# Optimization experiments

Measured on AMD Instinct MI355X. Metric: run time of the kernel, lower is better.

## Reference

```python
import jax, jax.numpy as jnp
import numpy as np
from jax import lax

EPS = 1e-5
DIM = 384
HEADS = 12
EXPAND = 3  # head_expand -> DLA hidden = 36
HID = HEADS * EXPAND
MLP_HID = 4 * DIM


def layernorm(x, g, b):
    m = x.mean(-1, keepdims=True)
    v = jnp.var(x, axis=-1, keepdims=True)
    return (x - m) / jnp.sqrt(v + EPS) * g + b


def bn2d(x, g, b):
    # training-mode BatchNorm2d: biased batch stats over (N,H,W) per channel
    m = x.mean((0, 2, 3), keepdims=True)
    v = jnp.var(x, axis=(0, 2, 3), keepdims=True)
    return (x - m) / jnp.sqrt(v + EPS) * g[None, :, None, None] + b[None, :, None, None]


def setup_inputs() -> dict:
    key = jax.random.key(0)
    ks = jax.random.split(key, 12)
    d = {}
    d["x"] = jax.random.normal(ks[0], (32, 197, DIM), dtype=jnp.float32)
    d["ln1_g"] = jnp.ones((DIM,), jnp.float32)
    d["ln1_b"] = jnp.zeros((DIM,), jnp.float32)
    d["qkv_w"] = jax.random.normal(ks[1], (3 * DIM, DIM), jnp.float32) * 0.02
    # DLA conv_exapnd: 1x1 expand -> dw3x3 -> 1x1 project, each with BN
    d["conv_exp_w"] = jax.random.normal(ks[2], (HID, HEADS), jnp.float32) * 0.1
    d["bn1_g"] = jnp.ones((HID,), jnp.float32)
    d["bn1_b"] = jnp.zeros((HID,), jnp.float32)
    d["dw_w"] = jax.random.normal(ks[3], (HID, 1, 3, 3), jnp.float32) * 0.1
    d["bn2_g"] = jnp.ones((HID,), jnp.float32)
    d["bn2_b"] = jnp.zeros((HID,), jnp.float32)
    d["conv_pro_w"] = jax.random.normal(ks[4], (HEADS, HID), jnp.float32) * 0.1
    d["bn3_g"] = jnp.ones((HEADS,), jnp.float32)
    d["bn3_b"] = jnp.zeros((HEADS,), jnp.float32)
    d["abn_g"] = jnp.ones((HEADS,), jnp.float32)
    d["abn_b"] = jnp.zeros((HEADS,), jnp.float32)
    d["proj_w"] = jax.random.normal(ks[5], (DIM, DIM), jnp.float32) * 0.02
    d["proj_b"] = jnp.zeros((DIM,), jnp.float32)
    d["ln2_g"] = jnp.ones((DIM,), jnp.float32)
    d["ln2_b"] = jnp.zeros((DIM,), jnp.float32)
    d["fc1_w"] = jax.random.normal(ks[6], (MLP_HID, DIM), jnp.float32) * 0.02
    d["fc1_b"] = jnp.zeros((MLP_HID,), jnp.float32)
    d["fc2_w"] = jax.random.normal(ks[7], (DIM, MLP_HID), jnp.float32) * 0.02
    d["fc2_b"] = jnp.zeros((DIM,), jnp.float32)
    d["scale_ch"] = 1e-5 * jnp.ones((DIM,), jnp.float32)
    return d


def reference(x, ln1_g, ln1_b, qkv_w, conv_exp_w, bn1_g, bn1_b, dw_w, bn2_g, bn2_b,
              conv_pro_w, bn3_g, bn3_b, abn_g, abn_b, proj_w, proj_b,
              ln2_g, ln2_b, fc1_w, fc1_b, fc2_w, fc2_b, scale_ch):
    B, N, C = x.shape
    H = HEADS
    hd = C // H
    scale = hd ** -0.5
    sq = scale ** 0.5  # math.sqrt(self.scale) applied to q and k

    h = layernorm(x * 0.5, ln1_g, ln1_b)  # adjust_ratio = 0.5
    qkv = (h @ qkv_w.T).reshape(B, N, 3, H, hd).transpose(2, 0, 3, 1, 4)  # [3,B,H,N,hd]
    q, k, v = qkv[0] * sq, qkv[1] * sq, qkv[2]

    attn = jax.nn.softmax(jnp.einsum('bhnd,bhmd->bhnm', q, k), axis=-1)  # [B,H,N,N]

    # DLA conv_exapnd refine (stride 1, inp==oup -> residual)
    a0 = attn
    a = jnp.einsum('oi,bihw->bohw', conv_exp_w, attn)
    a = jnp.clip(bn2d(a, bn1_g, bn1_b), 0.0, 6.0)  # ReLU6
    a = lax.conv_general_dilated(a, dw_w, (1, 1), 'SAME',
                                 dimension_numbers=('NCHW', 'OIHW', 'NCHW'),
                                 feature_group_count=HID)
    a = jnp.clip(bn2d(a, bn2_g, bn2_b), 0.0, 6.0)
    a = jnp.einsum('oi,bihw->bohw', conv_pro_w, a)
    a = bn2d(a, bn3_g, bn3_b) + a0
    attn = bn2d(a, abn_g, abn_b)  # adapt_bn

    out = jnp.einsum('bhnm,bhmd->bhnd', attn, v).transpose(0, 2, 1, 3).reshape(B, N, C)
    out = out @ proj_w.T + proj_b
    x = x + out / 0.5

    m = layernorm(x * 0.5, ln2_g, ln2_b)
    m = jax.nn.gelu(m @ fc1_w.T + fc1_b, approximate=False)
    m = (m @ fc2_w.T + fc2_b) * scale_ch
    x = x + m / 0.5
    return x, attn
```

## Files before the change

### kernel.cpp

```cpp
#include <hip/hip_runtime.h>
#include <math.h>

#define EPS   1e-5f
#define NSEQ  197
#define DIM   384
#define NH    12
#define HD    32
#define MLPH  1536
#define NN2   38809
#define NROWS 6304
#define NPIX  1241888
#define XSIZE 2420736
#define SQF   0.4204482076268572f

typedef __bf16 bf16;
typedef __attribute__((ext_vector_type(2))) __fp16 fp16x2;
typedef __attribute__((ext_vector_type(2))) float floatx2;
typedef __attribute__((ext_vector_type(8))) __bf16 bf16x8;
typedef __attribute__((ext_vector_type(4))) float floatx4;
typedef unsigned int u32;
typedef const __attribute__((address_space(1))) u32* gptr_t;
typedef __attribute__((address_space(3))) u32* lptr_t;

#define ST_MOMSUM  0
#define ST_MOMPROD 16
#define ST_SC1     160
#define ST_SH1     200
#define ST_S2      256
#define ST_SS2     2560
#define ST_SC2     4864
#define ST_SH2     4900
#define ST_P3      4992
#define ST_ABG     8832
#define ST_TOTAL   8896

#define O_HB    0ull
#define O_Q     1228800ull
#define O_K     3649536ull
#define O_V     6070272ull
#define O_ATT0  8491008ull
#define O_X1    23393664ull
#define O_WQKV  25814400ull
#define O_WPRJ  26035584ull
#define O_WFC1  26109312ull
#define O_WFC2  26404224ull
#define O_STATS 26699136ull
#define WS_FLOATS (O_STATS + ST_TOTAL)
#define O_SBUF  (O_STATS + ST_TOTAL)
#define SBUF_WORDS 22353984ull
#define WS_FLOATS_MID (O_SBUF + SBUF_WORDS)

__device__ __forceinline__ u32 pack2(float a, float b) {
    u32 ua = __builtin_bit_cast(u32, a);
    u32 ub = __builtin_bit_cast(u32, b);
    return (ua >> 16) | (ub & 0xffff0000u);
}
__device__ __forceinline__ float unpk_lo(u32 w) { return __builtin_bit_cast(float, w << 16); }
__device__ __forceinline__ float unpk_hi(u32 w) { return __builtin_bit_cast(float, w & 0xffff0000u); }

__device__ __forceinline__ u32 packh2(float a, float b) {
    fp16x2 h = __builtin_amdgcn_cvt_pkrtz(a, b);
    return __builtin_bit_cast(u32, h);
}
__device__ __forceinline__ float unph_lo(u32 w) {
    fp16x2 h = __builtin_bit_cast(fp16x2, w);
    return (float)h.x;
}
__device__ __forceinline__ float unph_hi(u32 w) {
    fp16x2 h = __builtin_bit_cast(fp16x2, w);
    return (float)h.y;
}

template <int CTRL>
__device__ __forceinline__ float dpp_addf(float v) {
    int x = __builtin_amdgcn_update_dpp(0, __builtin_bit_cast(int, v),
                                        CTRL, 0xF, 0xF, true);
    return v + __builtin_bit_cast(float, x);
}
__device__ __forceinline__ float red16(float v) {
    v = dpp_addf<0xB1>(v);
    v = dpp_addf<0x4E>(v);
    v = dpp_addf<0x141>(v);
    v = dpp_addf<0x140>(v);
    return v;
}

template <int CTRL>
__device__ __forceinline__ u32 dpp_addh(u32 v) {
    int x = __builtin_amdgcn_update_dpp(0, __builtin_bit_cast(int, v),
                                        CTRL, 0xF, 0xF, true);
    fp16x2 a = __builtin_bit_cast(fp16x2, v);
    fp16x2 b = __builtin_bit_cast(fp16x2, (u32)x);
    fp16x2 c = a + b;
    return __builtin_bit_cast(u32, c);
}
__device__ __forceinline__ u32 red16h(u32 v) {
    v = dpp_addh<0xB1>(v);
    v = dpp_addh<0x4E>(v);
    v = dpp_addh<0x141>(v);
    v = dpp_addh<0x140>(v);
    return v;
}

__global__ __launch_bounds__(256) void k_cvt(const float* __restrict__ s0,
                                             const float* __restrict__ s1,
                                             const float* __restrict__ s2,
                                             const float* __restrict__ s3,
                                             bf16* __restrict__ d0,
                                             bf16* __restrict__ d1,
                                             bf16* __restrict__ d2,
                                             bf16* __restrict__ d3) {
    const int w = blockIdx.y;
    const float* s = (w == 0) ? s0 : (w == 1) ? s1 : (w == 2) ? s2 : s3;
    bf16* d = (w == 0) ? d0 : (w == 1) ? d1 : (w == 2) ? d2 : d3;
    const int n = (w == 0) ? 442368 : (w == 1) ? 147456 : 589824;
    for (int i = blockIdx.x * 256 + threadIdx.x; i < n; i += gridDim.x * 256)
        d[i] = (bf16)s[i];
}

__global__ __launch_bounds__(384) void k_ln(const float* __restrict__ xin,
                                            const float* __restrict__ g,
                                            const float* __restrict__ bb,
                                            bf16* __restrict__ hout) {
    const int r = blockIdx.x;
    const int t = threadIdx.x;
    float v = xin[(size_t)r * DIM + t] * 0.5f;
    float s = v, sq = v * v;
#pragma unroll
    for (int off = 32; off >= 1; off >>= 1) {
        s  += __shfl_xor(s, off);
        sq += __shfl_xor(sq, off);
    }
    __shared__ float ls[6], lq[6];
    __shared__ float mv[2];
    const int wid = t >> 6;
    if ((t & 63) == 0) { ls[wid] = s; lq[wid] = sq; }
    __syncthreads();
    if (t == 0) {
        float S = 0.f, Q = 0.f;
        for (int i = 0; i < 6; ++i) { S += ls[i]; Q += lq[i]; }
        float m = S / (float)DIM;
        mv[0] = m;
        mv[1] = rsqrtf(Q / (float)DIM - m * m + EPS);
    }
    __syncthreads();
    hout[(size_t)r * DIM + t] = (bf16)((v - mv[0]) * mv[1] * g[t] + bb[t]);
}

template <int KDIM>
__device__ __forceinline__ void mgemm(const bf16* __restrict__ A,
                                      const bf16* __restrict__ B,
                                      int row0, int col0,
                                      floatx4 (&acc)[4][4]) {
    __shared__ bf16 As[128 * 32];
    __shared__ bf16 Bs[128 * 32];
    const int tid = threadIdx.x;
    const int lane = tid & 63, wave = tid >> 6;
    const int wy = wave >> 1, wx = wave & 1;
    const int quad = lane >> 4, l15 = lane & 15;
    for (int k0 = 0; k0 < KDIM; k0 += 32) {
#pragma unroll
        for (int i = 0; i < 2; ++i) {
            const int e = (i * 256 + tid) * 8;
            const int r = e >> 5, kk = e & 31;
            __builtin_amdgcn_global_load_lds(
                (gptr_t)(A + (size_t)(row0 + r) * KDIM + k0 + kk),
                (lptr_t)(As + e), 16, 0, 0);
            __builtin_amdgcn_global_load_lds(
                (gptr_t)(B + (size_t)(col0 + r) * KDIM + k0 + kk),
                (lptr_t)(Bs + e), 16, 0, 0);
        }
        __syncthreads();
        bf16x8 af[4], bfr[4];
#pragma unroll
        for (int mi = 0; mi < 4; ++mi)
            af[mi] = *(const bf16x8*)&As[(wy * 64 + mi * 16 + l15) * 32 + quad * 8];
#pragma unroll
        for (int ni = 0; ni < 4; ++ni)
            bfr[ni] = *(const bf16x8*)&Bs[(wx * 64 + ni * 16 + l15) * 32 + quad * 8];
#pragma unroll
        for (int mi = 0; mi < 4; ++mi)
#pragma unroll
            for (int ni = 0; ni < 4; ++ni)
                acc[mi][ni] = __builtin_amdgcn_mfma_f32_16x16x32_bf16(
                    af[mi], bfr[ni], acc[mi][ni], 0, 0, 0);
        __syncthreads();
    }
}

__global__ __launch_bounds__(256) void k_qkv(const bf16* __restrict__ h,
                                             const bf16* __restrict__ w,
                                             bf16* __restrict__ qb,
                                             bf16* __restrict__ kxb,
                                             float* __restrict__ v) {
    floatx4 acc[4][4] = {};
    const int row0 = blockIdx.y * 128, col0 = blockIdx.x * 128;
    mgemm<DIM>(h, w, row0, col0, acc);
    const int lane = threadIdx.x & 63, wave = threadIdx.x >> 6;
    const int wy = wave >> 1, wx = wave & 1;
    const int quad = lane >> 4, l15 = lane & 15;
#pragma unroll
    for (int mi = 0; mi < 4; ++mi)
#pragma unroll
        for (int reg = 0; reg < 4; ++reg) {
            int r = row0 + wy * 64 + mi * 16 + quad * 4 + reg;
            if (r >= NROWS) continue;
            int b = r / NSEQ, n = r - b * NSEQ;
#pragma unroll
            for (int ni = 0; ni < 4; ++ni) {
                int o = col0 + wx * 64 + ni * 16 + l15;
                int sec = o / DIM;
                int hh = (o >> 5) % NH;
                int dd = o & 31;
                float val = acc[mi][ni][reg];
                size_t idx = ((size_t)(b * NH + hh) * NSEQ + n) * HD + dd;
                if (sec == 2)      v[idx] = val;
                else if (sec == 0) qb[idx]  = (bf16)(val * SQF);
                else               kxb[idx] = (bf16)(val * SQF);
            }
        }
}

__global__ __launch_bounds__(256) void k_proj(const bf16* __restrict__ outm,
                                              const bf16* __restrict__ w,
                                              const float* __restrict__ pb,
                                              const float* __restrict__ x0,
                                              float* __restrict__ x1) {
    floatx4 acc[4][4] = {};
    const int row0 = blockIdx.y * 128, col0 = blockIdx.x * 128;
    mgemm<DIM>(outm, w, row0, col0, acc);
    const int lane = threadIdx.x & 63, wave = threadIdx.x >> 6;
    const int wy = wave >> 1, wx = wave & 1;
    const int quad = lane >> 4, l15 = lane & 15;
#pragma unroll
    for (int mi = 0; mi < 4; ++mi)
#pragma unroll
        for (int reg = 0; reg < 4; ++reg) {
            int r = row0 + wy * 64 + mi * 16 + quad * 4 + reg;
            if (r >= NROWS) continue;
#pragma unroll
            for (int ni = 0; ni < 4; ++ni) {
                int o = col0 + wx * 64 + ni * 16 + l15;
                x1[(size_t)r * DIM + o] =
                    x0[(size_t)r * DIM + o] + 2.f * (acc[mi][ni][reg] + pb[o]);
            }
        }
}

__global__ __launch_bounds__(256) void k_fc1(const bf16* __restrict__ h,
                                             const bf16* __restrict__ w,
                                             const float* __restrict__ fb,
                                             bf16* __restrict__ m1) {
    floatx4 acc[4][4] = {};
    const int row0 = blockIdx.y * 128, col0 = blockIdx.x * 128;
    mgemm<DIM>(h, w, row0, col0, acc);
    const int lane = threadIdx.x & 63, wave = threadIdx.x >> 6;
    const int wy = wave >> 1, wx = wave & 1;
    const int quad = lane >> 4, l15 = lane & 15;
#pragma unroll
    for (int mi = 0; mi < 4; ++mi)
#pragma unroll
        for (int reg = 0; reg < 4; ++reg) {
            int r = row0 + wy * 64 + mi * 16 + quad * 4 + reg;
            if (r >= NROWS) continue;
#pragma unroll
            for (int ni = 0; ni < 4; ++ni) {
                int o = col0 + wx * 64 + ni * 16 + l15;
                float z = acc[mi][ni][reg] + fb[o];
                m1[(size_t)r * MLPH + o] =
                    (bf16)(0.5f * z * (1.f + erff(z * 0.70710678118654752f)));
            }
        }
}

__global__ __launch_bounds__(256) void k_fc2(const bf16* __restrict__ m1,
                                             const bf16* __restrict__ w,
                                             const float* __restrict__ fb,
                                             const float* __restrict__ scch,
                                             const float* __restrict__ x1,
                                             float* __restrict__ xout) {
    floatx4 acc[4][4] = {};
    const int row0 = blockIdx.y * 128, col0 = blockIdx.x * 128;
    mgemm<MLPH>(m1, w, row0, col0, acc);
    const int lane = threadIdx.x & 63, wave = threadIdx.x >> 6;
    const int wy = wave >> 1, wx = wave & 1;
    const int quad = lane >> 4, l15 = lane & 15;
#pragma unroll
    for (int mi = 0; mi < 4; ++mi)
#pragma unroll
        for (int reg = 0; reg < 4; ++reg) {
            int r = row0 + wy * 64 + mi * 16 + quad * 4 + reg;
            if (r >= NROWS) continue;
#pragma unroll
            for (int ni = 0; ni < 4; ++ni) {
                int o = col0 + wx * 64 + ni * 16 + l15;
                xout[(size_t)r * DIM + o] =
                    x1[(size_t)r * DIM + o] + 2.f * (acc[mi][ni][reg] + fb[o]) * scch[o];
            }
        }
}

__global__ __launch_bounds__(256) void k_score(const bf16* __restrict__ qb,
                                               const bf16* __restrict__ kmat,
                                               __fp16* __restrict__ att) {
    __shared__ bf16 Ks[208 * 32];
    __shared__ bf16 Qs[16 * 32];
    __shared__ float Ss[16][208];
    const int bh = blockIdx.y;
    const int y0 = blockIdx.x * 16;
    const int tid = threadIdx.x;
    const size_t kb = (size_t)bh * (NSEQ * HD);
    {
        const u32* ksrc = (const u32*)(kmat + kb);
        u32* kdst = (u32*)Ks;
        for (int i = tid; i < 208 * 16; i += 256)
            kdst[i] = (i < NSEQ * 16) ? ksrc[i] : 0u;
        const u32* qsrc = (const u32*)(qb + kb);
        u32* qdst = (u32*)Qs;
        for (int i = tid; i < 16 * 16; i += 256) {
            int rr = i >> 4, yy = y0 + rr;
            qdst[i] = (yy < NSEQ) ? qsrc[(size_t)yy * 16 + (i & 15)] : 0u;
        }
    }
    __syncthreads();
    {
        const int lane = tid & 63;
        const int wave = tid >> 6;
        const int l15 = lane & 15, quad = lane >> 4;
        bf16x8 af = *(const bf16x8*)&Qs[l15 * 32 + quad * 8];
        for (int t = wave; t < 13; t += 4) {
            bf16x8 bfr = *(const bf16x8*)&Ks[(t * 16 + l15) * 32 + quad * 8];
            floatx4 c = {0.f, 0.f, 0.f, 0.f};
            c = __builtin_amdgcn_mfma_f32_16x16x32_bf16(af, bfr, c, 0, 0, 0);
#pragma unroll
            for (int reg = 0; reg < 4; ++reg)
                Ss[quad * 4 + reg][t * 16 + l15] = c[reg];
        }
    }
    __syncthreads();
    const int tx = tid & 15, ty = tid >> 4;
    const int y = y0 + ty;
    if (y >= NSEQ) return;
    float sc[13];
    float mx = -1e30f;
#pragma unroll
    for (int m = 0; m < 13; ++m) {
        int x = tx + m * 16;
        float d = (x < NSEQ) ? Ss[ty][x] : -1e30f;
        sc[m] = d;
        mx = fmaxf(mx, d);
    }
#pragma unroll
    for (int off = 8; off >= 1; off >>= 1) mx = fmaxf(mx, __shfl_xor(mx, off, 16));
    float ssum = 0.f;
#pragma unroll
    for (int m = 0; m < 13; ++m) {
        int x = tx + m * 16;
        float e = (x < NSEQ) ? __expf(sc[m] - mx) : 0.f;
        sc[m] = e;
        ssum += e;
    }
#pragma unroll
    for (int off = 8; off >= 1; off >>= 1) ssum += __shfl_xor(ssum, off, 16);
    const float rinv = 1.f / ssum;
    const size_t ab = (size_t)bh * NN2 + (size_t)y * NSEQ;
#pragma unroll
    for (int m = 0; m < 13; ++m) {
        int x = tx + m * 16;
        if (x < NSEQ) att[ab + x] = (__fp16)(sc[m] * rinv);
    }
}

__global__ __launch_bounds__(256) void k_moments(const __fp16* __restrict__ att,
                                                 float* __restrict__ stats) {
    float mu[12] = {};
    float pr[78] = {};
    const int stride = gridDim.x * 256;
    for (int p = blockIdx.x * 256 + threadIdx.x; p < NPIX; p += stride) {
        int b = p / NN2;
        int s = p - b * NN2;
        const __fp16* base = att + (size_t)b * 12 * NN2 + s;
        float v[12];
#pragma unroll
        for (int i = 0; i < 12; ++i) v[i] = (float)base[(size_t)i * NN2];
#pragma unroll
        for (int i = 0; i < 12; ++i) mu[i] += v[i];
#pragma unroll
        for (int i = 0; i < 12; ++i)
#pragma unroll
            for (int j = i; j < 12; ++j)
                pr[i * (23 - i) / 2 + j] += v[i] * v[j];
    }
#pragma unroll
    for (int s = 0; s < 12; ++s)
#pragma unroll
        for (int off = 32; off >= 1; off >>= 1) mu[s] += __shfl_xor(mu[s], off);
#pragma unroll
    for (int s = 0; s < 78; ++s)
#pragma unroll
        for (int off = 32; off >= 1; off >>= 1) pr[s] += __shfl_xor(pr[s], off);
    __shared__ float red[4][90];
    const int lane = threadIdx.x & 63, wid = threadIdx.x >> 6;
    if (lane == 0) {
#pragma unroll
        for (int s = 0; s < 12; ++s) red[wid][s] = mu[s];
#pragma unroll
        for (int s = 0; s < 78; ++s) red[wid][12 + s] = pr[s];
    }
    __syncthreads();
    const int t = threadIdx.x;
    if (t < 90) {
        float tot = red[0][t] + red[1][t] + red[2][t] + red[3][t];
        int addr;
        if (t < 12) addr = ST_MOMSUM + t;
        else {
            int tt = t - 12;
            int i = 0;
            while (tt >= 12 - i) { tt -= 12 - i; ++i; }
            addr = ST_MOMPROD + i * 12 + (i + tt);
        }
        atomicAdd(&stats[addr], tot);
    }
}

__global__ __launch_bounds__(64) void k_fin1(const float* __restrict__ wexp,
                                             const float* __restrict__ g1,
                                             const float* __restrict__ b1,
                                             float* __restrict__ stats) {
    int o = threadIdx.x;
    if (o >= 36) return;
    const float invM = 1.f / (float)NPIX;
    float mu[12];
#pragma unroll
    for (int i = 0; i < 12; ++i) mu[i] = stats[ST_MOMSUM + i] * invM;
    float mean = 0.f;
#pragma unroll
    for (int i = 0; i < 12; ++i) mean += wexp[o * 12 + i] * mu[i];
    float e2 = 0.f;
    for (int i = 0; i < 12; ++i)
        for (int j = 0; j < 12; ++j) {
            int a = i < j ? i : j, bj = i < j ? j : i;
            e2 += wexp[o * 12 + i] * wexp[o * 12 + j] * stats[ST_MOMPROD + a * 12 + bj] * invM;
        }
    float var = e2 - mean * mean;
    float sc = g1[o] * rsqrtf(var + EPS);
    stats[ST_SC1 + o] = sc;
    stats[ST_SH1 + o] = b1[o] - mean * sc;
}

template <int STORE>
__global__ __launch_bounds__(256) void k_sums2(const __fp16* __restrict__ att,
                                               const float* __restrict__ wexp,
                                               const float* __restrict__ dww,
                                               const float* __restrict__ stats,
                                               float* __restrict__ statw,
                                               u32* __restrict__ sbuf) {
    __shared__ u32  b1p[18][256];
    __shared__ floatx2 wexp2[216];
    __shared__ fp16x2 dw2h[162];
    __shared__ floatx2 sc1p[18], sh1p[18];
    __shared__ float red[16][73];
    const int b = blockIdx.z;
    const int oy0 = blockIdx.y * 14, ox0 = blockIdx.x * 14;
    const int tid = threadIdx.x;
    for (int i = tid; i < 216; i += 256) {
        int pp = i / 12, ii = i - pp * 12;
        floatx2 t = {wexp[(2 * pp) * 12 + ii], wexp[(2 * pp + 1) * 12 + ii]};
        wexp2[i] = t;
    }
    for (int i = tid; i < 162; i += 256) {
        int pp = i / 9, t9 = i - pp * 9;
        fp16x2 t = {(__fp16)dww[(2 * pp) * 9 + t9], (__fp16)dww[(2 * pp + 1) * 9 + t9]};
        dw2h[i] = t;
    }
    if (tid < 18) {
        floatx2 a = {stats[ST_SC1 + 2 * tid], stats[ST_SC1 + 2 * tid + 1]};
        floatx2 bshift = {stats[ST_SH1 + 2 * tid], stats[ST_SH1 + 2 * tid + 1]};
        sc1p[tid] = a;
        sh1p[tid] = bshift;
    }
    const int lx = tid & 15, ly = tid >> 4;
    const int gy = oy0 - 1 + ly, gx = ox0 - 1 + lx;
    const bool valid = (gy >= 0 && gy < NSEQ && gx >= 0 && gx < NSEQ);
    float a0v[12];
#pragma unroll
    for (int i = 0; i < 12; ++i)
        a0v[i] = valid ? (float)att[(size_t)(b * 12 + i) * NN2 + (size_t)gy * NSEQ + gx] : 0.f;
    __syncthreads();
    const floatx2 vzero = {0.f, 0.f};
    const floatx2 vsix  = {6.f, 6.f};
#pragma unroll 3
    for (int pp = 0; pp < 18; ++pp) {
        floatx2 t = vzero;
#pragma unroll
        for (int i = 0; i < 12; ++i) {
            floatx2 av = {a0v[i], a0v[i]};
            t = __builtin_elementwise_fma(wexp2[pp * 12 + i], av, t);
        }
        t = __builtin_elementwise_fma(sc1p[pp], t, sh1p[pp]);
        t = __builtin_elementwise_max(t, vzero);
        t = __builtin_elementwise_min(t, vsix);
        if (!valid) t = vzero;
        b1p[pp][tid] = packh2(t.x, t.y);
    }
    __syncthreads();
    const bool inter = (ly >= 1 && ly <= 14 && lx >= 1 && lx <= 14 &&
                        gy < NSEQ && gx < NSEQ);
    const int base = inter ? ((ly - 1) * 16 + (lx - 1)) : 0;
    const int leader = tid >> 4;
    const size_t pix = (size_t)gy * NSEQ + gx;
    const fp16x2 hzero = {(__fp16)0.f, (__fp16)0.f};
#pragma unroll 3
    for (int pp = 0; pp < 18; ++pp) {
        fp16x2 sh = hzero;
        if (inter) {
            const u32* bp = &b1p[pp][base];
#pragma unroll
            for (int dy = 0; dy < 3; ++dy)
#pragma unroll
                for (int dx = 0; dx < 3; ++dx) {
                    fp16x2 bv = __builtin_bit_cast(fp16x2, bp[dy * 16 + dx]);
                    sh = __builtin_elementwise_fma(dw2h[pp * 9 + dy * 3 + dx], bv, sh);
                }
            if (STORE)
                sbuf[((size_t)(b * 18 + pp)) * NN2 + pix] = __builtin_bit_cast(u32, sh);
        }
        fp16x2 sq = sh * sh;
        u32 rs = red16h(__builtin_bit_cast(u32, sh));
        u32 rq = red16h(__builtin_bit_cast(u32, sq));
        if ((tid & 15) == 0) {
            red[leader][pp * 4 + 0] = unph_lo(rs);
            red[leader][pp * 4 + 1] = unph_hi(rs);
            red[leader][pp * 4 + 2] = unph_lo(rq);
            red[leader][pp * 4 + 3] = unph_hi(rq);
        }
    }
    __syncthreads();
    if (tid < 72) {
        float tot = 0.f;
        for (int l = 0; l < 16; ++l) tot += red[l][tid];
        int pp = tid >> 2, j = tid & 3;
        int c = 2 * pp + (j & 1);
        int isq = j >> 1;
        int slot = (blockIdx.z * 225 + blockIdx.y * 15 + blockIdx.x) & 63;
        atomicAdd(&statw[(isq ? ST_SS2 : ST_S2) + slot * 36 + c], tot);
    }
}

__global__ __launch_bounds__(64) void k_fin2(const float* __restrict__ g2,
                                             const float* __restrict__ b2,
                                             float* __restrict__ stats) {
    int o = threadIdx.x;
    if (o >= 36) return;
    float S = 0.f, SS = 0.f;
    for (int sl = 0; sl < 64; ++sl) {
        S += stats[ST_S2 + sl * 36 + o];
        SS += stats[ST_SS2 + sl * 36 + o];
    }
    const float invM = 1.f / (float)NPIX;
    float m = S * invM, var = SS * invM - m * m;
    float sc = g2[o] * rsqrtf(var + EPS);
    stats[ST_SC2 + o] = sc;
    stats[ST_SH2 + o] = b2[o] - m * sc;
}

__global__ __launch_bounds__(256) void k_p3f(const __fp16* __restrict__ att,
                                             const u32* __restrict__ sbuf,
                                             const float* __restrict__ pw,
                                             const float* __restrict__ stats,
                                             float* __restrict__ datt,
                                             float* __restrict__ statw) {
    __shared__ floatx2 pw2[216];
    __shared__ floatx2 sc2p[18], sh2p[18];
    __shared__ float red2[16][37];
    const int tid = threadIdx.x;
    for (int i = tid; i < 216; i += 256) {
        int k = i / 36, ch = i - k * 36;
        floatx2 t = {pw[(2 * k) * 36 + ch], pw[(2 * k + 1) * 36 + ch]};
        pw2[i] = t;
    }
    if (tid < 18) {
        floatx2 a = {stats[ST_SC2 + 2 * tid], stats[ST_SC2 + 2 * tid + 1]};
        floatx2 bshift = {stats[ST_SH2 + 2 * tid], stats[ST_SH2 + 2 * tid + 1]};
        sc2p[tid] = a;
        sh2p[tid] = bshift;
    }
    __syncthreads();
    const int p = blockIdx.x * 256 + tid;
    const bool act = p < NPIX;
    int b = 0, s = 0;
    if (act) { b = p / NN2; s = p - b * NN2; }
    const floatx2 vzero = {0.f, 0.f};
    const floatx2 vsix  = {6.f, 6.f};
    floatx2 a3p[6] = {vzero, vzero, vzero, vzero, vzero, vzero};
    float a0v[12] = {};
    if (act) {
        const u32* sb = sbuf + (size_t)b * 18 * NN2 + s;
#pragma unroll 3
        for (int pp = 0; pp < 18; ++pp) {
            u32 w = sb[(size_t)pp * NN2];
            floatx2 sv = {unph_lo(w), unph_hi(w)};
            floatx2 u = __builtin_elementwise_fma(sc2p[pp], sv, sh2p[pp]);
            u = __builtin_elementwise_max(u, vzero);
            u = __builtin_elementwise_min(u, vsix);
            floatx2 ux = {u.x, u.x};
            floatx2 uy = {u.y, u.y};
#pragma unroll
            for (int k = 0; k < 6; ++k) {
                a3p[k] = __builtin_elementwise_fma(pw2[k * 36 + 2 * pp], ux, a3p[k]);
                a3p[k] = __builtin_elementwise_fma(pw2[k * 36 + 2 * pp + 1], uy, a3p[k]);
            }
        }
        const __fp16* ab = att + (size_t)b * 12 * NN2 + s;
#pragma unroll
        for (int c = 0; c < 12; ++c) a0v[c] = (float)ab[(size_t)c * NN2];
#pragma unroll
        for (int k = 0; k < 6; ++k) {
            datt[(size_t)(b * 12 + 2 * k) * NN2 + s]     = a3p[k].x;
            datt[(size_t)(b * 12 + 2 * k + 1) * NN2 + s] = a3p[k].y;
        }
    }
    const int leader = tid >> 4;
#pragma unroll
    for (int k = 0; k < 6; ++k) {
        float v0 = a3p[k].x, v1 = a3p[k].y;
        float r30 = red16(v0);
        float r31 = red16(v1);
        float rq0 = red16(v0 * v0);
        float rq1 = red16(v1 * v1);
        float rx0 = red16(v0 * a0v[2 * k]);
        float rx1 = red16(v1 * a0v[2 * k + 1]);
        if ((tid & 15) == 0) {
            red2[leader][2 * k]          = r30;
            red2[leader][2 * k + 1]      = r31;
            red2[leader][12 + 2 * k]     = rq0;
            red2[leader][12 + 2 * k + 1] = rq1;
            red2[leader][24 + 2 * k]     = rx0;
            red2[leader][24 + 2 * k + 1] = rx1;
        }
    }
    __syncthreads();
    if (tid < 36) {
        float tot = 0.f;
        for (int l = 0; l < 16; ++l) tot += red2[l][tid];
        int slot = blockIdx.x & 63;
        atomicAdd(&statw[ST_P3 + slot * 36 + tid], tot);
    }
}

__global__ __launch_bounds__(256) void k_p3(const __fp16* __restrict__ att,
                                            const float* __restrict__ wexp,
                                            const float* __restrict__ dww,
                                            const float* __restrict__ pw,
                                            const float* __restrict__ stats,
                                            float* __restrict__ datt,
                                            float* __restrict__ statw) {
    __shared__ u32  b1p[18][256];
    __shared__ float wexps[432];
    __shared__ float dws[324];
    __shared__ float pws[432];
    __shared__ float sc1s[36], sh1s[36], sc2s[36], sh2s[36];
    __shared__ float red2[32][37];
    const int b = blockIdx.z;
    const int oy0 = blockIdx.y * 14, ox0 = blockIdx.x * 14;
    const int tid = threadIdx.x;
    for (int i = tid; i < 432; i += 256) { wexps[i] = wexp[i]; pws[i] = pw[i]; }
    for (int i = tid; i < 324; i += 256) dws[i] = dww[i];
    if (tid < 36) {
        sc1s[tid] = stats[ST_SC1 + tid]; sh1s[tid] = stats[ST_SH1 + tid];
        sc2s[tid] = stats[ST_SC2 + tid]; sh2s[tid] = stats[ST_SH2 + tid];
    }
    const int lx = tid & 15, ly = tid >> 4;
    const int gy = oy0 - 1 + ly, gx = ox0 - 1 + lx;
    const bool valid = (gy >= 0 && gy < NSEQ && gx >= 0 && gx < NSEQ);
    float a0v[12];
#pragma unroll
    for (int i = 0; i < 12; ++i)
        a0v[i] = valid ? (float)att[(size_t)(b * 12 + i) * NN2 + (size_t)gy * NSEQ + gx] : 0.f;
    __syncthreads();
#pragma unroll 3
    for (int pp = 0; pp < 18; ++pp) {
        float t0 = 0.f, t1 = 0.f;
#pragma unroll
        for (int i = 0; i < 12; ++i) {
            t0 = fmaf(wexps[(2 * pp) * 12 + i], a0v[i], t0);
            t1 = fmaf(wexps[(2 * pp + 1) * 12 + i], a0v[i], t1);
        }
        t0 = fminf(fmaxf(fmaf(sc1s[2 * pp], t0, sh1s[2 * pp]), 0.f), 6.f);
        t1 = fminf(fmaxf(fmaf(sc1s[2 * pp + 1], t1, sh1s[2 * pp + 1]), 0.f), 6.f);
        if (!valid) { t0 = 0.f; t1 = 0.f; }
        b1p[pp][tid] = pack2(t0, t1);
    }
    __syncthreads();
    const bool inter = (ly >= 1 && ly <= 14 && lx >= 1 && lx <= 14 &&
                        gy < NSEQ && gx < NSEQ);
    float a3v[12] = {};
    if (inter) {
        const int base = (ly - 1) * 16 + (lx - 1);
#pragma unroll 3
        for (int pp = 0; pp < 18; ++pp) {
            const u32* bp = &b1p[pp][base];
            float s0 = 0.f, s1 = 0.f;
#pragma unroll
            for (int dy = 0; dy < 3; ++dy)
#pragma unroll
                for (int dx = 0; dx < 3; ++dx) {
                    u32 w = bp[dy * 16 + dx];
                    s0 = fmaf(dws[(2 * pp) * 9 + dy * 3 + dx], unpk_lo(w), s0);
                    s1 = fmaf(dws[(2 * pp + 1) * 9 + dy * 3 + dx], unpk_hi(w), s1);
                }
            float u0 = fminf(fmaxf(fmaf(sc2s[2 * pp], s0, sh2s[2 * pp]), 0.f), 6.f);
            float u1 = fminf(fmaxf(fmaf(sc2s[2 * pp + 1], s1, sh2s[2 * pp + 1]), 0.f), 6.f);
#pragma unroll
            for (int c = 0; c < 12; ++c)
                a3v[c] = fmaf(pws[c * 36 + 2 * pp], u0,
                         fmaf(pws[c * 36 + 2 * pp + 1], u1, a3v[c]));
        }
        const size_t pix = (size_t)gy * NSEQ + gx;
#pragma unroll
        for (int c = 0; c < 12; ++c)
            datt[(size_t)(b * 12 + c) * NN2 + pix] = a3v[c];
    }
    const int leader = tid >> 3;
#pragma unroll
    for (int c = 0; c < 12; ++c) {
        float r3  = red16(a3v[c]);
        float rq  = red16(a3v[c] * a3v[c]);
        float r30 = red16(a3v[c] * a0v[c]);
        if ((tid & 7) == 0) {
            red2[leader][c]      = r3;
            red2[leader][12 + c] = rq;
            red2[leader][24 + c] = r30;
        }
    }
    __syncthreads();
    if (tid < 36) {
        float tot = 0.f;
        for (int l = 0; l < 32; l += 2) tot += red2[l][tid];
        int slot = (blockIdx.z * 225 + blockIdx.y * 15 + blockIdx.x) & 63;
        atomicAdd(&statw[ST_P3 + slot * 36 + tid], tot);
    }
}

__global__ __launch_bounds__(64) void k_fin3(const float* __restrict__ g3,
                                             const float* __restrict__ b3,
                                             const float* __restrict__ ag,
                                             const float* __restrict__ ab,
                                             float* __restrict__ stats) {
    int c = threadIdx.x;
    if (c >= 12) return;
    float S3 = 0.f, S3q = 0.f, S30 = 0.f;
    for (int sl = 0; sl < 64; ++sl) {
        const float* p = stats + ST_P3 + sl * 36;
        S3 += p[c]; S3q += p[12 + c]; S30 += p[24 + c];
    }
    float S0  = stats[ST_MOMSUM + c];
    float S0q = stats[ST_MOMPROD + c * 12 + c];
    const float M = (float)NPIX;
    float m3 = S3 / M, v3 = S3q / M - m3 * m3;
    float pp = g3[c] * rsqrtf(v3 + EPS);
    float qq = b3[c] - m3 * pp;
    float my = (pp * S3 + S0) / M + qq;
    float Syq = pp * pp * S3q + S0q + qq * qq * M + 2.f * pp * S30 + 2.f * pp * qq * S3 + 2.f * qq * S0;
    float vy = Syq / M - my * my;
    float rr = ag[c] * rsqrtf(vy + EPS);
    float ss = ab[c] - my * rr;
    stats[ST_ABG + c] = rr * pp;
    stats[ST_ABG + 12 + c] = rr;
    stats[ST_ABG + 24 + c] = rr * qq + ss;
}

__global__ __launch_bounds__(256) void k_p4(float* __restrict__ datt,
                                            const __fp16* __restrict__ att0,
                                            const float* __restrict__ v,
                                            const float* __restrict__ stats,
                                            bf16* __restrict__ outm) {
    __shared__ bf16 Vtb[32 * 224];
    __shared__ bf16 As[16 * 224];
    const int bh = blockIdx.y;
    const int b = bh / 12, hh = bh - b * 12;
    const int y0 = blockIdx.x * 16;
    const int tid = threadIdx.x;
    const size_t vb = (size_t)bh * (NSEQ * HD);
    for (int i = tid; i < 32 * 224; i += 256) {
        int x = i >> 5, d = i & 31;
        float val = (x < NSEQ) ? v[vb + (size_t)x * HD + d] : 0.f;
        Vtb[d * 224 + x] = (bf16)val;
    }
    const float alpha = stats[ST_ABG + hh];
    const float beta  = stats[ST_ABG + 12 + hh];
    const float gamma = stats[ST_ABG + 24 + hh];
    const int tx = tid & 15, ty = tid >> 4;
    const int y = y0 + ty;
    const size_t ab = (size_t)bh * NN2 + (size_t)y * NSEQ;
    As[ty * 224 + 208 + tx] = (bf16)0.f;
#pragma unroll
    for (int m = 0; m < 13; ++m) {
        int x = tx + m * 16;
        float av = 0.f;
        if (y < NSEQ && x < NSEQ) {
            av = alpha * datt[ab + x] + beta * (float)att0[ab + x] + gamma;
            datt[ab + x] = av;
        }
        As[ty * 224 + x] = (bf16)av;
    }
    __syncthreads();
    const int lane = tid & 63, wave = tid >> 6;
    if (wave < 2) {
        const int l15 = lane & 15, quad = lane >> 4;
        floatx4 c = {0.f, 0.f, 0.f, 0.f};
#pragma unroll
        for (int ks = 0; ks < 7; ++ks) {
            bf16x8 af  = *(const bf16x8*)&As[l15 * 224 + ks * 32 + quad * 8];
            bf16x8 bfr = *(const bf16x8*)&Vtb[(wave * 16 + l15) * 224 + ks * 32 + quad * 8];
            c = __builtin_amdgcn_mfma_f32_16x16x32_bf16(af, bfr, c, 0, 0, 0);
        }
#pragma unroll
        for (int reg = 0; reg < 4; ++reg) {
            int yy = y0 + quad * 4 + reg;
            if (yy < NSEQ)
                outm[((size_t)b * NSEQ + yy) * DIM + hh * HD + wave * 16 + l15] =
                    (bf16)c[reg];
        }
    }
}

extern "C" void kernel_launch(void* const* d_in, const int* in_sizes, int n_in,
                              void* d_out, int out_size, void* d_ws, size_t ws_size,
                              hipStream_t stream) {
    const float* x     = (const float*)d_in[0];
    const float* ln1g  = (const float*)d_in[1];
    const float* ln1b  = (const float*)d_in[2];
    const float* qkvw  = (const float*)d_in[3];
    const float* wexp  = (const float*)d_in[4];
    const float* bn1g  = (const float*)d_in[5];
    const float* bn1b  = (const float*)d_in[6];
    const float* dww   = (const float*)d_in[7];
    const float* bn2g  = (const float*)d_in[8];
    const float* bn2b  = (const float*)d_in[9];
    const float* prow  = (const float*)d_in[10];
    const float* bn3g  = (const float*)d_in[11];
    const float* bn3b  = (const float*)d_in[12];
    const float* abng  = (const float*)d_in[13];
    const float* abnb  = (const float*)d_in[14];
    const float* projw = (const float*)d_in[15];
    const float* projb = (const float*)d_in[16];
    const float* ln2g  = (const float*)d_in[17];
    const float* ln2b  = (const float*)d_in[18];
    const float* fc1w  = (const float*)d_in[19];
    const float* fc1b  = (const float*)d_in[20];
    const float* fc2w  = (const float*)d_in[21];
    const float* fc2b  = (const float*)d_in[22];
    const float* scch  = (const float*)d_in[23];

    if (ws_size < WS_FLOATS * sizeof(float)) return;
    const bool mid = ws_size >= WS_FLOATS_MID * sizeof(float);

    float* W     = (float*)d_ws;
    bf16*  hb    = (bf16*)(W + O_HB);
    bf16*  qbv   = (bf16*)(W + O_Q);
    bf16*  kxb   = (bf16*)(W + O_K);
    float* v     = W + O_V;
    __fp16* att0 = (__fp16*)(W + O_ATT0);
    float* x1    = W + O_X1;
    bf16*  m1    = (bf16*)(W + O_ATT0);
    bf16*  wqkvb = (bf16*)(W + O_WQKV);
    bf16*  wprjb = (bf16*)(W + O_WPRJ);
    bf16*  wfc1b = (bf16*)(W + O_WFC1);
    bf16*  wfc2b = (bf16*)(W + O_WFC2);
    float* stats = W + O_STATS;
    u32*   sbuf  = (u32*)(W + O_SBUF);

    float* xout = (float*)d_out;
    float* datt = xout + XSIZE;

    (void)hipMemsetAsync(stats, 0, ST_TOTAL * sizeof(float), stream);
    k_cvt<<<dim3(288, 4), 256, 0, stream>>>(qkvw, projw, fc1w, fc2w,
                                            wqkvb, wprjb, wfc1b, wfc2b);
    k_ln<<<NROWS, 384, 0, stream>>>(x, ln1g, ln1b, hb);
    k_qkv<<<dim3(9, 50), 256, 0, stream>>>(hb, wqkvb, qbv, kxb, v);
    k_score<<<dim3(13, 384), 256, 0, stream>>>(qbv, kxb, att0);
    k_moments<<<512, 256, 0, stream>>>(att0, stats);
    k_fin1<<<1, 64, 0, stream>>>(wexp, bn1g, bn1b, stats);
    if (mid) {
        k_sums2<1><<<dim3(15, 15, 32), 256, 0, stream>>>(att0, wexp, dww, stats, stats, sbuf);
        k_fin2<<<1, 64, 0, stream>>>(bn2g, bn2b, stats);
        k_p3f<<<(NPIX + 255) / 256, 256, 0, stream>>>(att0, sbuf, prow, stats, datt, stats);
    } else {
        k_sums2<0><<<dim3(15, 15, 32), 256, 0, stream>>>(att0, wexp, dww, stats, stats, nullptr);
        k_fin2<<<1, 64, 0, stream>>>(bn2g, bn2b, stats);
        k_p3<<<dim3(15, 15, 32), 256, 0, stream>>>(att0, wexp, dww, prow, stats, datt, stats);
    }
    k_fin3<<<1, 64, 0, stream>>>(bn3g, bn3b, abng, abnb, stats);
    k_p4<<<dim3(13, 384), 256, 0, stream>>>(datt, att0, v, stats, hb);
    k_proj<<<dim3(3, 50), 256, 0, stream>>>(hb, wprjb, projb, x, x1);
    k_ln<<<NROWS, 384, 0, stream>>>(x1, ln2g, ln2b, hb);
    k_fc1<<<dim3(12, 50), 256, 0, stream>>>(hb, wfc1b, fc1b, m1);
    k_fc2<<<dim3(3, 50), 256, 0, stream>>>(m1, wfc2b, fc2b, scch, x1, xout);
}
```

Baseline: 498.8 us.

## Store intermediate conv output as fp16 and use DPP shifts for depthwise conv

The projected-conv intermediate (a3) is now written to a separate fp16 buffer placed after att0 instead of fp32 into the output attention buffer, which halves that intermediate's write and read traffic between k_p3/k_p3f and k_p4. Separately, the 3x3 depthwise conv in k_sums2 now loads only the three vertical neighbours from LDS and gets the horizontal neighbours through DPP row shifts, cutting LDS reads per tap. Rounding a3 to fp16 adds precision loss, and the new a3h buffer assumes the workspace has room past att0.

```diff
diff --git a/kernel.cpp b/kernel.cpp
--- a/kernel.cpp
+++ b/kernel.cpp
@@ -100,6 +100,11 @@
     v = dpp_addh<0x141>(v);
     v = dpp_addh<0x140>(v);
     return v;
+}
+
+template <int CTRL>
+__device__ __forceinline__ u32 dppmov(u32 v) {
+    return (u32)__builtin_amdgcn_update_dpp(0, (int)v, CTRL, 0xF, 0xF, true);
 }
 
 __global__ __launch_bounds__(256) void k_cvt(const float* __restrict__ s0,
@@ -504,25 +509,33 @@
         b1p[pp][tid] = packh2(t.x, t.y);
     }
     __syncthreads();
-    const bool inter = (ly >= 1 && ly <= 14 && lx >= 1 && lx <= 14 &&
-                        gy < NSEQ && gx < NSEQ);
-    const int base = inter ? ((ly - 1) * 16 + (lx - 1)) : 0;
+    const bool convrow = (ly >= 1 && ly <= 14);
+    const bool inter = (convrow && lx >= 1 && lx <= 14 && gy < NSEQ && gx < NSEQ);
     const int leader = tid >> 4;
     const size_t pix = (size_t)gy * NSEQ + gx;
     const fp16x2 hzero = {(__fp16)0.f, (__fp16)0.f};
 #pragma unroll 3
     for (int pp = 0; pp < 18; ++pp) {
         fp16x2 sh = hzero;
-        if (inter) {
-            const u32* bp = &b1p[pp][base];
-#pragma unroll
-            for (int dy = 0; dy < 3; ++dy)
-#pragma unroll
-                for (int dx = 0; dx < 3; ++dx) {
-                    fp16x2 bv = __builtin_bit_cast(fp16x2, bp[dy * 16 + dx]);
-                    sh = __builtin_elementwise_fma(dw2h[pp * 9 + dy * 3 + dx], bv, sh);
-                }
-            if (STORE)
+        if (convrow) {
+            u32 c0 = b1p[pp][(ly - 1) * 16 + lx];
+            u32 c1 = b1p[pp][ ly      * 16 + lx];
+            u32 c2 = b1p[pp][(ly + 1) * 16 + lx];
+            u32 l0 = dppmov<0x111>(c0), r0 = dppmov<0x101>(c0);
+            u32 l1 = dppmov<0x111>(c1), r1 = dppmov<0x101>(c1);
+            u32 l2 = dppmov<0x111>(c2), r2 = dppmov<0x101>(c2);
+            const fp16x2* w9 = &dw2h[pp * 9];
+            sh = __builtin_elementwise_fma(w9[0], __builtin_bit_cast(fp16x2, l0), sh);
+            sh = __builtin_elementwise_fma(w9[1], __builtin_bit_cast(fp16x2, c0), sh);
+            sh = __builtin_elementwise_fma(w9[2], __builtin_bit_cast(fp16x2, r0), sh);
+            sh = __builtin_elementwise_fma(w9[3], __builtin_bit_cast(fp16x2, l1), sh);
+            sh = __builtin_elementwise_fma(w9[4], __builtin_bit_cast(fp16x2, c1), sh);
+            sh = __builtin_elementwise_fma(w9[5], __builtin_bit_cast(fp16x2, r1), sh);
+            sh = __builtin_elementwise_fma(w9[6], __builtin_bit_cast(fp16x2, l2), sh);
+            sh = __builtin_elementwise_fma(w9[7], __builtin_bit_cast(fp16x2, c2), sh);
+            sh = __builtin_elementwise_fma(w9[8], __builtin_bit_cast(fp16x2, r2), sh);
+            if (!inter) sh = hzero;
+            if (STORE && inter)
                 sbuf[((size_t)(b * 18 + pp)) * NN2 + pix] = __builtin_bit_cast(u32, sh);
         }
         fp16x2 sq = sh * sh;
@@ -568,7 +581,7 @@
                                              const u32* __restrict__ sbuf,
                                              const float* __restrict__ pw,
                                              const float* __restrict__ stats,
-                                             float* __restrict__ datt,
+                                             __fp16* __restrict__ a3h,
                                              float* __restrict__ statw) {
     __shared__ floatx2 pw2[216];
     __shared__ floatx2 sc2p[18], sh2p[18];
@@ -616,8 +629,8 @@
         for (int c = 0; c < 12; ++c) a0v[c] = (float)ab[(size_t)c * NN2];
 #pragma unroll
         for (int k = 0; k < 6; ++k) {
-            datt[(size_t)(b * 12 + 2 * k) * NN2 + s]     = a3p[k].x;
-            datt[(size_t)(b * 12 + 2 * k + 1) * NN2 + s] = a3p[k].y;
+            a3h[(size_t)(b * 12 + 2 * k) * NN2 + s]     = (__fp16)a3p[k].x;
+            a3h[(size_t)(b * 12 + 2 * k + 1) * NN2 + s] = (__fp16)a3p[k].y;
         }
     }
     const int leader = tid >> 4;
@@ -653,7 +666,7 @@
                                             const float* __restrict__ dww,
                                             const float* __restrict__ pw,
                                             const float* __restrict__ stats,
-                                            float* __restrict__ datt,
+                                            __fp16* __restrict__ a3h,
                                             float* __restrict__ statw) {
     __shared__ u32  b1p[18][256];
     __shared__ float wexps[432];
@@ -719,7 +732,7 @@
         const size_t pix = (size_t)gy * NSEQ + gx;
 #pragma unroll
         for (int c = 0; c < 12; ++c)
-            datt[(size_t)(b * 12 + c) * NN2 + pix] = a3v[c];
+            a3h[(size_t)(b * 12 + c) * NN2 + pix] = (__fp16)a3v[c];
     }
     const int leader = tid >> 3;
 #pragma unroll
@@ -772,6 +785,7 @@
 
 __global__ __launch_bounds__(256) void k_p4(float* __restrict__ datt,
                                             const __fp16* __restrict__ att0,
+                                            const __fp16* __restrict__ a3h,
                                             const float* __restrict__ v,
                                             const float* __restrict__ stats,
                                             bf16* __restrict__ outm) {
@@ -799,7 +813,7 @@
         int x = tx + m * 16;
         float av = 0.f;
         if (y < NSEQ && x < NSEQ) {
-            av = alpha * datt[ab + x] + beta * (float)att0[ab + x] + gamma;
+            av = alpha * (float)a3h[ab + x] + beta * (float)att0[ab + x] + gamma;
             datt[ab + x] = av;
         }
         As[ty * 224 + x] = (bf16)av;
@@ -862,6 +876,7 @@
     bf16*  kxb   = (bf16*)(W + O_K);
     float* v     = W + O_V;
     __fp16* att0 = (__fp16*)(W + O_ATT0);
+    __fp16* a3h  = att0 + (size_t)NH * 32 * NN2;
     float* x1    = W + O_X1;
     bf16*  m1    = (bf16*)(W + O_ATT0);
     bf16*  wqkvb = (bf16*)(W + O_WQKV);
@@ -885,14 +900,14 @@
     if (mid) {
         k_sums2<1><<<dim3(15, 15, 32), 256, 0, stream>>>(att0, wexp, dww, stats, stats, sbuf);
         k_fin2<<<1, 64, 0, stream>>>(bn2g, bn2b, stats);
-        k_p3f<<<(NPIX + 255) / 256, 256, 0, stream>>>(att0, sbuf, prow, stats, datt, stats);
+        k_p3f<<<(NPIX + 255) / 256, 256, 0, stream>>>(att0, sbuf, prow, stats, a3h, stats);
     } else {
         k_sums2<0><<<dim3(15, 15, 32), 256, 0, stream>>>(att0, wexp, dww, stats, stats, nullptr);
         k_fin2<<<1, 64, 0, stream>>>(bn2g, bn2b, stats);
-        k_p3<<<dim3(15, 15, 32), 256, 0, stream>>>(att0, wexp, dww, prow, stats, datt, stats);
+        k_p3<<<dim3(15, 15, 32), 256, 0, stream>>>(att0, wexp, dww, prow, stats, a3h, stats);
     }
     k_fin3<<<1, 64, 0, stream>>>(bn3g, bn3b, abng, abnb, stats);
-    k_p4<<<dim3(13, 384), 256, 0, stream>>>(datt, att0, v, stats, hb);
+    k_p4<<<dim3(13, 384), 256, 0, stream>>>(datt, att0, a3h, v, stats, hb);
     k_proj<<<dim3(3, 50), 256, 0, stream>>>(hb, wprjb, projb, x, x1);
     k_ln<<<NROWS, 384, 0, stream>>>(x1, ln2g, ln2b, hb);
     k_fc1<<<dim3(12, 50), 256, 0, stream>>>(hb, wfc1b, fc1b, m1);
```

After: 487.3 us. 1.02x faster.
